# Kernel tuning notes

Measured on AMD Instinct MI355X. Metric: run time of the kernel, lower is better.

Reference implementation:

```python
import jax, jax.numpy as jnp
import numpy as np

N_UNITS = 512
N_HEADS = 8
CHUNK = N_UNITS // N_HEADS
SCALE = 1.0 / (CHUNK ** 0.5)


def setup_inputs() -> dict:
    key = jax.random.key(0)
    k1, k2, k3, k4, k5, k6 = jax.random.split(key, 6)
    B, Nx, Ny = 8, 1024, 1024
    x = jax.random.normal(k1, (B, N_UNITS, Nx), dtype=jnp.float32)
    y = jax.random.normal(k2, (B, N_UNITS, Ny), dtype=jnp.float32)
    xy_mask = jax.random.randint(k3, (B, Nx, Ny), 0, 2) > 0
    # conv1x1 weight [out, in] (ConvolutionSentence, bias=False)
    W = jax.random.normal(k4, (N_UNITS, N_UNITS), dtype=jnp.float32) * (1.0 / np.sqrt(N_UNITS))
    fc_w = jax.random.normal(k5, (1, N_HEADS), dtype=jnp.float32) * (1.0 / np.sqrt(N_HEADS))
    fc_b = jax.random.normal(k6, (1,), dtype=jnp.float32) * 0.01
    return {"x": x, "y": y, "xy_mask": xy_mask, "W": W, "fc_w": fc_w, "fc_b": fc_b}


def reference(x, y, xy_mask, W, fc_w, fc_b):
    B, U, Nx = x.shape
    Ny = y.shape[2]
    H, C = N_HEADS, CHUNK
    # 1x1 conv over channel dim == linear on channels
    _x = jnp.einsum('oi,bin->bon', W, x)  # [B, U, Nx]
    _y = jnp.einsum('oi,bim->bom', W, y)  # [B, U, Ny]
    # split channels into heads (contiguous chunks, matching torch.split)
    xh = _x.reshape(B, H, C, Nx)
    yh = _y.reshape(B, H, C, Ny)
    # per-head scores: relu, then scale, then mask (order matches torch code)
    s = jnp.einsum('bhcn,bhcm->bhnm', xh, yh)  # [B, H, Nx, Ny]
    s = jnp.maximum(s, 0.0) * SCALE
    s = jnp.where(xy_mask[:, None, :, :], s, 0.0)
    similarity = s.sum(axis=(2, 3))  # [B, H]
    n_el = xy_mask.sum(axis=(1, 2))
    n_el = jnp.where(n_el == 0, 1, n_el).astype(similarity.dtype)
    expectation = similarity / n_el[:, None]
    return expectation @ fc_w.T + fc_b  # [B, 1]
```

## Files before the change

kernel.cpp:

```cpp
#include <hip/hip_runtime.h>
#include <stdint.h>

#define UU 512
#define NHEAD 8
#define NB 8
#define NXX 1024
#define NYY 1024
#define SCALE_F 0.125f

typedef __bf16 bf16x8 __attribute__((ext_vector_type(8)));
typedef float f32x4 __attribute__((ext_vector_type(4)));
typedef unsigned short us4 __attribute__((ext_vector_type(4)));

__device__ __forceinline__ unsigned short f2bf(float f) {
  union { float f; uint32_t u; } v; v.f = f;
  return (unsigned short)((v.u + 0x7FFFu + ((v.u >> 16) & 1u)) >> 16);
}

__global__ void prep_kernel(const float* __restrict__ W, unsigned short* __restrict__ Wp,
                            const unsigned char* __restrict__ m, int* __restrict__ det) {
  int blk = blockIdx.x, t = threadIdx.x;
  if (blk < 128) {
    int s = blk * 256 + t;
    int ub = s >> 10, kb = (s >> 6) & 15, l = s & 63;
    int u = ub * 16 + (l & 15), k = kb * 32 + (l >> 4) * 8;
    const float* src = W + (size_t)u * UU + k;
    float4 a = *(const float4*)src;
    float4 bq = *(const float4*)(src + 4);
    uint4 o;
    o.x = (unsigned)f2bf(a.x) | ((unsigned)f2bf(a.y) << 16);
    o.y = (unsigned)f2bf(a.z) | ((unsigned)f2bf(a.w) << 16);
    o.z = (unsigned)f2bf(bq.x) | ((unsigned)f2bf(bq.y) << 16);
    o.w = (unsigned)f2bf(bq.z) | ((unsigned)f2bf(bq.w) << 16);
    *(uint4*)(Wp + (size_t)s * 8) = o;
  } else {
    int idx = ((blk - 128) * 256 + t) * 16;
    uint4 v = *(const uint4*)(m + idx);
    unsigned int c1 = (v.x & 0xff00u) | (v.y & 0xff00u) | (v.z & 0xff00u) | (v.w & 0xff00u);
    if (c1) atomicOr(&det[0], 1);
  }
}

__global__ __launch_bounds__(256, 2) void conv_fused(
    const float* __restrict__ x, const float* __restrict__ y,
    const unsigned short* __restrict__ Wp, unsigned short* __restrict__ cv) {
  __shared__ unsigned short xs[64 * 512];
  int fl = blockIdx.x;
  int bz = fl & 15, nt = (fl >> 4) & 15, ut = fl >> 8;
  int b = bz & 7;
  const float* src = (bz >> 3) ? y : x;
  int n0 = nt * 64;
  int t = threadIdx.x, w = t >> 6, l = t & 63;
  int lane_m = l & 15, lane_g = l >> 4;

  {
    int cq = (t & 15) * 4;
    int i2b = (t >> 4) * 2;
    const float* gb = src + (size_t)b * UU * NXX + n0 + cq;
#pragma unroll
    for (int it = 0; it < 16; it++) {
      int i2 = i2b + it * 32;
      float4 va = *(const float4*)(gb + (size_t)i2 * NXX);
      float4 vb = *(const float4*)(gb + (size_t)(i2 + 1) * NXX);
      float fa[4] = {va.x, va.y, va.z, va.w};
      float fb[4] = {vb.x, vb.y, vb.z, vb.w};
#pragma unroll
      for (int j = 0; j < 4; j++) {
        int n = cq + j;
        unsigned int pk = (unsigned)f2bf(fa[j]) | ((unsigned)f2bf(fb[j]) << 16);
        int e = n * 512 + (i2 ^ ((n & 7) << 3));
        *(unsigned int*)&xs[e] = pk;
      }
    }
  }
  __syncthreads();

  int u0 = ut * 256 + w * 64;
  int ub0 = u0 >> 4;
  const unsigned short* wb0 = Wp + (size_t)l * 8;
  f32x4 acc[4][4] = {};
  bf16x8 aA[4], aB[4], bA[4], bB[4];

#define LOADW(Adst, Bdst, KB) do {                                            \
    _Pragma("unroll") for (int tu = 0; tu < 4; tu++)                          \
      Adst[tu] = *(const bf16x8*)(wb0 + ((size_t)(ub0 + tu) * 16 + (KB)) * 512); \
    _Pragma("unroll") for (int tn = 0; tn < 4; tn++) {                        \
      int nl_ = tn * 16 + lane_m;                                             \
      int ka_ = (KB) * 32 + lane_g * 8;                                       \
      Bdst[tn] = *(const bf16x8*)&xs[nl_ * 512 + (ka_ ^ ((nl_ & 7) << 3))];   \
    }                                                                         \
  } while (0)
#define DOMFMA(Ab, Bb) do {                                                   \
    _Pragma("unroll") for (int tn = 0; tn < 4; tn++)                          \
    _Pragma("unroll") for (int tu = 0; tu < 4; tu++)                          \
      acc[tn][tu] = __builtin_amdgcn_mfma_f32_16x16x32_bf16(Ab[tu], Bb[tn], acc[tn][tu], 0, 0, 0); \
  } while (0)

  LOADW(aA, bA, 0);
#pragma unroll
  for (int kp = 0; kp < 8; kp++) {
    LOADW(aB, bB, 2 * kp + 1);
    DOMFMA(aA, bA);
    if (kp < 7) LOADW(aA, bA, 2 * kp + 2);
    DOMFMA(aB, bB);
  }
#undef LOADW
#undef DOMFMA

  unsigned short* ob = cv + (size_t)bz * NXX * UU;
#pragma unroll
  for (int tn = 0; tn < 4; tn++)
#pragma unroll
    for (int tu = 0; tu < 4; tu++) {
      int n = n0 + tn * 16 + lane_m;
      int u = u0 + tu * 16 + 4 * lane_g;
      us4 pk;
      pk.x = f2bf(acc[tn][tu][0]); pk.y = f2bf(acc[tn][tu][1]);
      pk.z = f2bf(acc[tn][tu][2]); pk.w = f2bf(acc[tn][tu][3]);
      *(us4*)(ob + (size_t)n * UU + u) = pk;
    }
}

__global__ __launch_bounds__(256, 2) void score_kernel(
    const unsigned short* __restrict__ cv, const void* __restrict__ maskp,
    const int* __restrict__ det, float* __restrict__ part) {
  __shared__ unsigned short ys[64 * 512];
  __shared__ unsigned short mf16[64][72];
  __shared__ float red[4][8];
  int fl = blockIdx.x;
  int b = fl & 7, rr = fl >> 3;
  int nt = rr & 15, mt = rr >> 4;
  int t = threadIdx.x, w = t >> 6, l = t & 63;
  int lane_m = l & 15, lane_g = l >> 4;
  int n0 = nt * 64, m0 = mt * 64;
  int nw0 = (w & 1) * 32, hq = (w >> 1) * 4;

  const unsigned short* xb = cv + ((size_t)b * NXX + n0 + nw0) * UU;
  bf16x8 afr[4][2][2];
#pragma unroll
  for (int hh = 0; hh < 4; hh++) {
    int co = (hq + hh) * 64;
#pragma unroll
    for (int tn = 0; tn < 2; tn++)
#pragma unroll
      for (int kb = 0; kb < 2; kb++)
        afr[hh][tn][kb] = *(const bf16x8*)(xb + (size_t)(tn * 16 + lane_m) * UU + co + kb * 32 + lane_g * 8);
  }

  const unsigned short* yb = cv + ((size_t)(NB + b) * NYY + m0) * UU;
  {
    int seg = t & 63;
#pragma unroll
    for (int p = 0; p < 16; p++) {
      int r2 = p * 4 + (t >> 6);
      uint4 v = *(const uint4*)(yb + (size_t)r2 * UU + seg * 8);
      int sp = seg ^ (r2 & 7);
      *(uint4*)&ys[r2 * 512 + sp * 8] = v;
    }
  }

  int is_u8 = det[0] != 0;
  unsigned int cl = 0;
  {
    int row = t >> 2, cq = (t & 3) * 16;
    size_t eb = ((size_t)b * NXX + n0 + row) * NYY + m0 + cq;
    if (is_u8) {
      uint4 v = *(const uint4*)((const unsigned char*)maskp + eb);
#pragma unroll
      for (int j = 0; j < 16; j++) {
        unsigned int word = ((const unsigned int*)&v)[j >> 2];
        int bit = ((word >> ((j & 3) * 8)) & 0xffu) != 0;
        mf16[row][cq + j] = bit ? 0x3F80u : 0u;
        cl += (unsigned)bit;
      }
    } else {
      const unsigned int* mp = (const unsigned int*)maskp + eb;
#pragma unroll
      for (int q = 0; q < 4; q++) {
        uint4 v = *(const uint4*)(mp + q * 4);
        unsigned int wds[4] = {v.x, v.y, v.z, v.w};
#pragma unroll
        for (int j = 0; j < 4; j++) {
          int bit = wds[j] != 0;
          mf16[row][cq + q * 4 + j] = bit ? 0x3F80u : 0u;
          cl += (unsigned)bit;
        }
      }
    }
  }
  for (int s = 1; s < 64; s <<= 1) cl += __shfl_xor(cl, s);
  if (l == 0) red[w][4] = (float)cl;
  __syncthreads();

  float mreg[2][4][4];
#pragma unroll
  for (int tn = 0; tn < 2; tn++)
#pragma unroll
    for (int tm = 0; tm < 4; tm++)
#pragma unroll
      for (int r = 0; r < 4; r++) {
        unsigned int u = (unsigned int)mf16[nw0 + tn * 16 + 4 * lane_g + r][tm * 16 + lane_m] << 16;
        union { unsigned int u; float f; } cvt; cvt.u = u;
        mreg[tn][tm][r] = cvt.f;
      }

  float hsv[4] = {0.f, 0.f, 0.f, 0.f};
#pragma unroll
  for (int hh = 0; hh < 4; hh++) {
    int segbase = (hq + hh) * 8;
    bf16x8 bfr[4][2];
#pragma unroll
    for (int tm = 0; tm < 4; tm++) {
      int row = tm * 16 + lane_m;
#pragma unroll
      for (int kb = 0; kb < 2; kb++) {
        int sp = (segbase + kb * 4 + lane_g) ^ (row & 7);
        bfr[tm][kb] = *(const bf16x8*)&ys[row * 512 + sp * 8];
      }
    }
#pragma unroll
    for (int tn = 0; tn < 2; tn++)
#pragma unroll
      for (int tm = 0; tm < 4; tm++) {
        f32x4 acc = {};
        acc = __builtin_amdgcn_mfma_f32_16x16x32_bf16(afr[hh][tn][0], bfr[tm][0], acc, 0, 0, 0);
        acc = __builtin_amdgcn_mfma_f32_16x16x32_bf16(afr[hh][tn][1], bfr[tm][1], acc, 0, 0, 0);
#pragma unroll
        for (int r = 0; r < 4; r++) {
          float v = acc[r];
          v = v > 0.f ? v : 0.f;
          hsv[hh] = fmaf(v, mreg[tn][tm][r], hsv[hh]);
        }
      }
  }
#pragma unroll
  for (int hh = 0; hh < 4; hh++) {
    float hs = hsv[hh];
    for (int s = 1; s < 64; s <<= 1) hs += __shfl_xor(hs, s);
    if (l == 0) red[w][hh] = hs;
  }
  __syncthreads();
  float* pb = part + (size_t)fl * 16;
  if (t < 8) {
    int q = t >> 2, hh = t & 3;
    pb[t] = red[q * 2][hh] + red[q * 2 + 1][hh];
  } else if (t == 8) {
    pb[8] = red[0][4] + red[1][4] + red[2][4] + red[3][4];
  }
}

__global__ __launch_bounds__(256) void finalize(
    const float* __restrict__ part, const float* __restrict__ fcw,
    const float* __restrict__ fcb, float* __restrict__ out) {
  __shared__ float red[4][9];
  int b = blockIdx.x;
  int t = threadIdx.x, w = t >> 6, l = t & 63;
  const float* pb = part + (size_t)(t * 8 + b) * 16;
  float v[9];
#pragma unroll
  for (int j = 0; j < 9; j++) v[j] = pb[j];
#pragma unroll
  for (int j = 0; j < 9; j++) {
    float s = v[j];
    for (int ss = 1; ss < 64; ss <<= 1) s += __shfl_xor(s, ss);
    v[j] = s;
  }
  if (l == 0)
#pragma unroll
    for (int j = 0; j < 9; j++) red[w][j] = v[j];
  __syncthreads();
  if (t == 0) {
    float s = 0.f, cn = 0.f;
#pragma unroll
    for (int h = 0; h < NHEAD; h++)
      s += (red[0][h] + red[1][h] + red[2][h] + red[3][h]) * fcw[h];
    cn = red[0][8] + red[1][8] + red[2][8] + red[3][8];
    if (cn < 0.5f) cn = 1.f;
    out[b] = s * (SCALE_F / cn) + fcb[0];
  }
}

extern "C" void kernel_launch(void* const* d_in, const int* in_sizes, int n_in,
                              void* d_out, int out_size, void* d_ws, size_t ws_size,
                              hipStream_t stream) {
  const float* x = (const float*)d_in[0];
  const float* y = (const float*)d_in[1];
  const void* mask = d_in[2];
  const float* W = (const float*)d_in[3];
  const float* fcw = (const float*)d_in[4];
  const float* fcb = (const float*)d_in[5];
  float* out = (float*)d_out;
  char* ws = (char*)d_ws;

  unsigned short* cv = (unsigned short*)ws;
  unsigned short* Wp = (unsigned short*)(ws + (16u << 20));
  float* part = (float*)(ws + (16u << 20) + (1u << 19));
  char* st = ws + (16u << 20) + (1u << 19) + (1u << 17);
  int* det = (int*)st;

  hipMemsetAsync(st, 0, 64, stream);
  prep_kernel<<<144, 256, 0, stream>>>(W, Wp, (const unsigned char*)mask, det);
  conv_fused<<<512, 256, 0, stream>>>(x, y, Wp, cv);
  score_kernel<<<2048, 256, 0, stream>>>(cv, mask, det, part);
  finalize<<<NB, 256, 0, stream>>>(part, fcw, fcb, out);
}
```

Measured before the change: 144.3 us.

## Store conv output in MFMA fragment-packed layout and drop score LDS staging

The conv kernel now writes its bf16 output in a layout packed per 16-row tile, head and k-block, so each lane's 8-element MFMA operand is contiguous. The score kernel then loads both x and y fragments straight from global memory with coalesced 16-byte loads instead of staging y through a 64 KB LDS tile. This removes the shared buffer and the swizzled LDS traffic, and raises the occupancy hint to 3 blocks per SM. In exchange, y fragments are re-read from global or L2 by every wave that needs them rather than being shared through LDS.

```diff
diff --git a/kernel.cpp b/kernel.cpp
--- a/kernel.cpp
+++ b/kernel.cpp
@@ -43,7 +43,7 @@
 
 __global__ __launch_bounds__(256, 2) void conv_fused(
     const float* __restrict__ x, const float* __restrict__ y,
-    const unsigned short* __restrict__ Wp, unsigned short* __restrict__ cv) {
+    const unsigned short* __restrict__ Wp, unsigned short* __restrict__ pc) {
   __shared__ unsigned short xs[64 * 512];
   int fl = blockIdx.x;
   int bz = fl & 15, nt = (fl >> 4) & 15, ut = fl >> 8;
@@ -107,24 +107,27 @@
 #undef LOADW
 #undef DOMFMA
 
-  unsigned short* ob = cv + (size_t)bz * NXX * UU;
+  unsigned short* ob = pc + (size_t)bz * 64 * 8 * 2 * 512;
+  int h = u0 >> 6;
+  int e0 = 4 * (lane_g & 1);
 #pragma unroll
   for (int tn = 0; tn < 4; tn++)
 #pragma unroll
     for (int tu = 0; tu < 4; tu++) {
-      int n = n0 + tn * 16 + lane_m;
-      int u = u0 + tu * 16 + 4 * lane_g;
+      int q16 = nt * 4 + tn;
+      int kb = tu >> 1;
+      int g = (2 * tu + (lane_g >> 1)) & 3;
+      size_t slot = ((size_t)q16 * 8 + h) * 2 + kb;
       us4 pk;
       pk.x = f2bf(acc[tn][tu][0]); pk.y = f2bf(acc[tn][tu][1]);
       pk.z = f2bf(acc[tn][tu][2]); pk.w = f2bf(acc[tn][tu][3]);
-      *(us4*)(ob + (size_t)n * UU + u) = pk;
+      *(us4*)(ob + slot * 512 + (g * 16 + lane_m) * 8 + e0) = pk;
     }
 }
 
-__global__ __launch_bounds__(256, 2) void score_kernel(
-    const unsigned short* __restrict__ cv, const void* __restrict__ maskp,
+__global__ __launch_bounds__(256, 3) void score_kernel(
+    const unsigned short* __restrict__ pc, const void* __restrict__ maskp,
     const int* __restrict__ det, float* __restrict__ part) {
-  __shared__ unsigned short ys[64 * 512];
   __shared__ unsigned short mf16[64][72];
   __shared__ float red[4][8];
   int fl = blockIdx.x;
@@ -135,30 +138,6 @@
   int n0 = nt * 64, m0 = mt * 64;
   int nw0 = (w & 1) * 32, hq = (w >> 1) * 4;
 
-  const unsigned short* xb = cv + ((size_t)b * NXX + n0 + nw0) * UU;
-  bf16x8 afr[4][2][2];
-#pragma unroll
-  for (int hh = 0; hh < 4; hh++) {
-    int co = (hq + hh) * 64;
-#pragma unroll
-    for (int tn = 0; tn < 2; tn++)
-#pragma unroll
-      for (int kb = 0; kb < 2; kb++)
-        afr[hh][tn][kb] = *(const bf16x8*)(xb + (size_t)(tn * 16 + lane_m) * UU + co + kb * 32 + lane_g * 8);
-  }
-
-  const unsigned short* yb = cv + ((size_t)(NB + b) * NYY + m0) * UU;
-  {
-    int seg = t & 63;
-#pragma unroll
-    for (int p = 0; p < 16; p++) {
-      int r2 = p * 4 + (t >> 6);
-      uint4 v = *(const uint4*)(yb + (size_t)r2 * UU + seg * 8);
-      int sp = seg ^ (r2 & 7);
-      *(uint4*)&ys[r2 * 512 + sp * 8] = v;
-    }
-  }
-
   int is_u8 = det[0] != 0;
   unsigned int cl = 0;
   {
@@ -204,27 +183,32 @@
         mreg[tn][tm][r] = cvt.f;
       }
 
+  int xq0 = (n0 + nw0) >> 4;
+  int yq0 = m0 >> 4;
+  const unsigned short* xpl = pc + ((size_t)b * 64) * 8 * 2 * 512 + (size_t)l * 8;
+  const unsigned short* ypl = pc + ((size_t)(NB + b) * 64) * 8 * 2 * 512 + (size_t)l * 8;
   float hsv[4] = {0.f, 0.f, 0.f, 0.f};
 #pragma unroll
   for (int hh = 0; hh < 4; hh++) {
-    int segbase = (hq + hh) * 8;
-    bf16x8 bfr[4][2];
-#pragma unroll
-    for (int tm = 0; tm < 4; tm++) {
-      int row = tm * 16 + lane_m;
-#pragma unroll
-      for (int kb = 0; kb < 2; kb++) {
-        int sp = (segbase + kb * 4 + lane_g) ^ (row & 7);
-        bfr[tm][kb] = *(const bf16x8*)&ys[row * 512 + sp * 8];
-      }
-    }
+    int h = hq + hh;
+    bf16x8 afr[2][2], bfr[4][2];
+#pragma unroll
+    for (int tn = 0; tn < 2; tn++)
+#pragma unroll
+      for (int kb = 0; kb < 2; kb++)
+        afr[tn][kb] = *(const bf16x8*)(xpl + ((((size_t)(xq0 + tn)) * 8 + h) * 2 + kb) * 512);
+#pragma unroll
+    for (int tm = 0; tm < 4; tm++)
+#pragma unroll
+      for (int kb = 0; kb < 2; kb++)
+        bfr[tm][kb] = *(const bf16x8*)(ypl + ((((size_t)(yq0 + tm)) * 8 + h) * 2 + kb) * 512);
 #pragma unroll
     for (int tn = 0; tn < 2; tn++)
 #pragma unroll
       for (int tm = 0; tm < 4; tm++) {
         f32x4 acc = {};
-        acc = __builtin_amdgcn_mfma_f32_16x16x32_bf16(afr[hh][tn][0], bfr[tm][0], acc, 0, 0, 0);
-        acc = __builtin_amdgcn_mfma_f32_16x16x32_bf16(afr[hh][tn][1], bfr[tm][1], acc, 0, 0, 0);
+        acc = __builtin_amdgcn_mfma_f32_16x16x32_bf16(afr[tn][0], bfr[tm][0], acc, 0, 0, 0);
+        acc = __builtin_amdgcn_mfma_f32_16x16x32_bf16(afr[tn][1], bfr[tm][1], acc, 0, 0, 0);
 #pragma unroll
         for (int r = 0; r < 4; r++) {
           float v = acc[r];
@@ -292,7 +276,7 @@
   float* out = (float*)d_out;
   char* ws = (char*)d_ws;
 
-  unsigned short* cv = (unsigned short*)ws;
+  unsigned short* pc = (unsigned short*)ws;
   unsigned short* Wp = (unsigned short*)(ws + (16u << 20));
   float* part = (float*)(ws + (16u << 20) + (1u << 19));
   char* st = ws + (16u << 20) + (1u << 19) + (1u << 17);
@@ -300,7 +284,7 @@
 
   hipMemsetAsync(st, 0, 64, stream);
   prep_kernel<<<144, 256, 0, stream>>>(W, Wp, (const unsigned char*)mask, det);
-  conv_fused<<<512, 256, 0, stream>>>(x, y, Wp, cv);
-  score_kernel<<<2048, 256, 0, stream>>>(cv, mask, det, part);
+  conv_fused<<<512, 256, 0, stream>>>(x, y, Wp, pc);
+  score_kernel<<<2048, 256, 0, stream>>>(pc, mask, det, part);
   finalize<<<NB, 256, 0, stream>>>(part, fcw, fcb, out);
 }
```

After: 142.5 us. No clear change (-1.2%).
